# Optimization experiments

Hardware: AMD Instinct MI355X
Metric: run time of the kernel (lower is better)

## Reference

```python
import jax, jax.numpy as jnp
import numpy as np
import math

N_HEAD = 8
N_FEAT = 512
D_K = N_FEAT // N_HEAD
B, T = 4, 2048


def setup_inputs() -> dict:
    key = jax.random.key(0)
    ks = jax.random.split(key, 16)
    s = 1.0 / math.sqrt(N_FEAT)
    return {
        "x": jax.random.normal(ks[0], (B, T, N_FEAT), dtype=jnp.float32),
        "pos_emb": jax.random.normal(ks[1], (1, T, N_FEAT), dtype=jnp.float32),
        "Wq": jax.random.normal(ks[2], (N_FEAT, N_FEAT), dtype=jnp.float32) * s,
        "bq": jnp.zeros((N_FEAT,), dtype=jnp.float32),
        "Wk": jax.random.normal(ks[3], (N_FEAT, N_FEAT), dtype=jnp.float32) * s,
        "bk": jnp.zeros((N_FEAT,), dtype=jnp.float32),
        "Wv": jax.random.normal(ks[4], (N_FEAT, N_FEAT), dtype=jnp.float32) * s,
        "bv": jnp.zeros((N_FEAT,), dtype=jnp.float32),
        "Wpos": jax.random.normal(ks[5], (N_FEAT, N_FEAT), dtype=jnp.float32) * s,
        "Wout": jax.random.normal(ks[6], (N_FEAT, N_FEAT), dtype=jnp.float32) * s,
        "bout": jnp.zeros((N_FEAT,), dtype=jnp.float32),
        "pos_bias_u": jax.random.normal(ks[7], (N_HEAD, D_K), dtype=jnp.float32) * 0.05,
        "pos_bias_v": jax.random.normal(ks[8], (N_HEAD, D_K), dtype=jnp.float32) * 0.05,
    }


def reference(x, pos_emb, Wq, bq, Wk, bk, Wv, bv, Wpos, Wout, bout,
              pos_bias_u, pos_bias_v):
    b, t, f = x.shape
    h, d = N_HEAD, D_K
    # QKV projections (torch Linear: y = x @ W.T + b), split into heads -> (B,H,T,d)
    q = (jnp.einsum('btf,of->bto', x, Wq) + bq).reshape(b, t, h, d).transpose(0, 2, 1, 3)
    k = (jnp.einsum('btf,of->bto', x, Wk) + bk).reshape(b, t, h, d).transpose(0, 2, 1, 3)
    v = (jnp.einsum('btf,of->bto', x, Wv) + bv).reshape(b, t, h, d).transpose(0, 2, 1, 3)
    # positional projection: (1, T_pos, F) -> (H, T_pos, d)
    tp = pos_emb.shape[1]
    p = jnp.einsum('ptf,of->pto', pos_emb, Wpos).reshape(tp, h, d).transpose(1, 0, 2)
    q_u = q + pos_bias_u[None, :, None, :]  # (B,H,T,d)
    q_v = q + pos_bias_v[None, :, None, :]
    matrix_ac = jnp.einsum('bhtd,bhsd->bhts', q_u, k)   # content-content
    matrix_bd = jnp.einsum('bhtd,hsd->bhts', q_v, p)    # content-position
    scores = (matrix_ac + matrix_bd) / math.sqrt(d)
    attn = jax.nn.softmax(scores, axis=-1)  # dropout is identity in eval mode
    out = jnp.einsum('bhts,bhsd->bhtd', attn, v)
    out = out.transpose(0, 2, 1, 3).reshape(b, t, h * d)
    return jnp.einsum('btf,of->bto', out, Wout) + bout
```

## Files before the change

### kernel.cpp

```cpp
#include <hip/hip_runtime.h>

typedef float f4 __attribute__((ext_vector_type(4)));
typedef __attribute__((ext_vector_type(8))) short bf16x8;
typedef __attribute__((ext_vector_type(4))) float f32x4;
typedef __attribute__((ext_vector_type(2))) int i32x2;

#define T_SEQ 2048
#define NFEAT 512
#define NHEAD 8
#define DK    64
#define BATCH 4

using gptr_t = const __attribute__((address_space(1))) void*;
using lptr_t = __attribute__((address_space(3))) void*;

#define LOG2E_8 0.18033688011f


static __device__ __forceinline__ short f2bf(float f) {
    unsigned u = __builtin_bit_cast(unsigned, f);
    u += 0x7fff + ((u >> 16) & 1);
    return (short)(u >> 16);
}
static __device__ __forceinline__ float b2f(short s) {
    unsigned u = ((unsigned)(unsigned short)s) << 16;
    return __builtin_bit_cast(float, u);
}
static __device__ __forceinline__ int pkbf(float a, float b) {
    unsigned ua = __builtin_bit_cast(unsigned, a) + 0x8000u;
    unsigned ub = __builtin_bit_cast(unsigned, b) + 0x8000u;
    return (int)((ua >> 16) | (ub & 0xFFFF0000u));
}

__global__ __launch_bounds__(256) void cvt_kernel(
    const float* __restrict__ x, const float* __restrict__ pos,
    const float* __restrict__ Wq, const float* __restrict__ Wk, const float* __restrict__ Wv,
    const float* __restrict__ Wpos, const float* __restrict__ Wout,
    const float* __restrict__ bq, const float* __restrict__ bk, const float* __restrict__ bv,
    short* __restrict__ xb, short* __restrict__ posb, short* __restrict__ wqkv,
    short* __restrict__ wpb, short* __restrict__ wob, float* __restrict__ bqkv)
{
    const int blk = blockIdx.x;
    const float* src; short* dst; int off;
    if      (blk < 2048) { src = x;    dst = xb;          off = blk * 2048; }
    else if (blk < 2560) { src = pos;  dst = posb;        off = (blk - 2048) * 2048; }
    else if (blk < 2688) { src = Wq;   dst = wqkv;        off = (blk - 2560) * 2048; }
    else if (blk < 2816) { src = Wk;   dst = wqkv + 262144; off = (blk - 2688) * 2048; }
    else if (blk < 2944) { src = Wv;   dst = wqkv + 524288; off = (blk - 2816) * 2048; }
    else if (blk < 3072) { src = Wpos; dst = wpb;         off = (blk - 2944) * 2048; }
    else if (blk < 3200) { src = Wout; dst = wob;         off = (blk - 3072) * 2048; }
    else {
        int t = threadIdx.x;
        bqkv[t]        = bq[t];        bqkv[256 + t]  = bq[256 + t];
        bqkv[512 + t]  = bk[t];        bqkv[768 + t]  = bk[256 + t];
        bqkv[1024 + t] = bv[t];        bqkv[1280 + t] = bv[256 + t];
        return;
    }
    int i = off + threadIdx.x * 8;
    f4 a = *(const f4*)(src + i);
    f4 b = *(const f4*)(src + i + 4);
    bf16x8 o;
#pragma unroll
    for (int j = 0; j < 4; ++j) { o[j] = f2bf(a[j]); o[4 + j] = f2bf(b[j]); }
    *(bf16x8*)(dst + i) = o;
}

template<int OUT_BF16>
static __device__ __forceinline__ void gemm_tile(
    short* As, short* Bs,
    const short* __restrict__ A, const short* __restrict__ B,
    const float* __restrict__ bias, void* __restrict__ Cv,
    int N, int K, int row0, int col0)
{
    const int tid = threadIdx.x, lane = tid & 63, wave = tid >> 6;
    const int col = lane & 15, quad = lane >> 4;
    const int wm = (wave >> 1) * 64, wn = (wave & 1) * 64;
    const int rl = lane & 15;

    const short* Abase = A + (size_t)(row0 + wave * 32 + rl) * K + (lane >> 4) * 8;
    const short* Bbase = B + (size_t)(col0 + wave * 32 + rl) * K + (lane >> 4) * 8;

    f32x4 acc[4][4];
#pragma unroll
    for (int i = 0; i < 4; ++i)
#pragma unroll
        for (int j = 0; j < 4; ++j) acc[i][j] = (f32x4){0.f, 0.f, 0.f, 0.f};

    for (int k0 = 0; k0 < K; k0 += 64) {
        __syncthreads();
#pragma unroll
        for (int c = 0; c < 2; ++c)
#pragma unroll
            for (int hf = 0; hf < 2; ++hf) {
                __builtin_amdgcn_global_load_lds((gptr_t)(Abase + (size_t)(16 * c) * K + k0 + hf * 32),
                                                 (lptr_t)(As + wave * 2048 + c * 1024 + hf * 512), 16, 0, 0);
                __builtin_amdgcn_global_load_lds((gptr_t)(Bbase + (size_t)(16 * c) * K + k0 + hf * 32),
                                                 (lptr_t)(Bs + wave * 2048 + c * 1024 + hf * 512), 16, 0, 0);
            }
        __syncthreads();
#pragma unroll
        for (int kt = 0; kt < 2; ++kt) {
            bf16x8 af[4], bfr[4];
#pragma unroll
            for (int mt = 0; mt < 4; ++mt)
                af[mt] = *(const bf16x8*)&As[((wm >> 4) + mt) * 1024 + (kt * 4 + quad) * 128 + col * 8];
#pragma unroll
            for (int nt = 0; nt < 4; ++nt)
                bfr[nt] = *(const bf16x8*)&Bs[((wn >> 4) + nt) * 1024 + (kt * 4 + quad) * 128 + col * 8];
#pragma unroll
            for (int mt = 0; mt < 4; ++mt)
#pragma unroll
                for (int nt = 0; nt < 4; ++nt)
                    acc[mt][nt] = __builtin_amdgcn_mfma_f32_16x16x32_bf16(af[mt], bfr[nt], acc[mt][nt], 0, 0, 0);
        }
    }

    float bv4[4];
#pragma unroll
    for (int nt = 0; nt < 4; ++nt)
        bv4[nt] = bias ? bias[col0 + wn + nt * 16 + col] : 0.f;
#pragma unroll
    for (int mt = 0; mt < 4; ++mt)
#pragma unroll
        for (int reg = 0; reg < 4; ++reg) {
            int r = row0 + wm + mt * 16 + quad * 4 + reg;
#pragma unroll
            for (int nt = 0; nt < 4; ++nt) {
                int c = col0 + wn + nt * 16 + col;
                float v = acc[mt][nt][reg] + bv4[nt];
                if (OUT_BF16) ((short*)Cv)[(size_t)r * N + c] = f2bf(v);
                else          ((float*)Cv)[(size_t)r * N + c] = v;
            }
        }
}

__global__ __launch_bounds__(256) void gemm_qkv_pos(
    const short* __restrict__ xb, const short* __restrict__ wqkv,
    const float* __restrict__ bqkv, short* __restrict__ QKV,
    const short* __restrict__ posb, const short* __restrict__ wpb,
    short* __restrict__ Pm)
{
    __shared__ short As[8192], Bs[8192];
    const int bid = blockIdx.x;
    if (bid < 768) {
        const int xcd = bid & 7, s = bid >> 3;
        const int row = xcd * 8 + (s & 7), colt = s >> 3;
        gemm_tile<1>(As, Bs, xb, wqkv, bqkv, QKV, 1536, 512, row * 128, colt * 128);
    } else {
        const int t = bid - 768;
        gemm_tile<1>(As, Bs, posb, wpb, nullptr, Pm, 512, 512, (t / 4) * 128, (t % 4) * 128);
    }
}

__global__ __launch_bounds__(256) void gemm_out_kernel(
    const short* __restrict__ Op, const float* __restrict__ Lb,
    const short* __restrict__ B, const float* __restrict__ bias,
    float* __restrict__ C)
{
    __shared__ short As[8192], Bs[8192];
    const int bid = blockIdx.x;
    const int xcd = bid & 7, s = bid >> 3;
    const int row0 = (xcd * 8 + (s & 7)) * 128, col0 = (s >> 3) * 128;
    const int N = 512, K = 512;

    const int tid = threadIdx.x, lane = tid & 63, wave = tid >> 6;
    const int col = lane & 15, quad = lane >> 4;
    const int wm = (wave >> 1) * 64, wn = (wave & 1) * 64;
    const int rl = lane & 15;

    const short* Bbase = B + (size_t)(col0 + wave * 32 + rl) * K + quad * 8;
    const int rA0 = row0 + wave * 32 + rl;

    f32x4 acc[4][4];
#pragma unroll
    for (int i = 0; i < 4; ++i)
#pragma unroll
        for (int j = 0; j < 4; ++j) acc[i][j] = (f32x4){0.f, 0.f, 0.f, 0.f};

    for (int k0 = 0; k0 < K; k0 += 64) {
        const int h = k0 >> 6;
        __syncthreads();
#pragma unroll
        for (int c = 0; c < 2; ++c)
#pragma unroll
            for (int hf = 0; hf < 2; ++hf)
                __builtin_amdgcn_global_load_lds((gptr_t)(Bbase + (size_t)(16 * c) * K + k0 + hf * 32),
                                                 (lptr_t)(Bs + wave * 2048 + c * 1024 + hf * 512), 16, 0, 0);
#pragma unroll
        for (int c = 0; c < 2; ++c) {
            const int r  = rA0 + c * 16;
            const int t  = r & 2047;
            const int bh = (r >> 11) * 8 + h;
            const float l = Lb[bh * T_SEQ + t] + Lb[65536 + bh * T_SEQ + t];
            const float inv = 1.f / l;
#pragma unroll
            for (int hf = 0; hf < 2; ++hf) {
                const short* src = Op + (size_t)r * NFEAT + k0 + hf * 32 + quad * 8;
                bf16x8 o1 = *(const bf16x8*)src;
                bf16x8 o2 = *(const bf16x8*)(src + 4194304);
                bf16x8 oc;
#pragma unroll
                for (int j = 0; j < 8; ++j) oc[j] = f2bf((b2f(o1[j]) + b2f(o2[j])) * inv);
                *(bf16x8*)&As[wave * 2048 + c * 1024 + hf * 512 + lane * 8] = oc;
            }
        }
        __syncthreads();
#pragma unroll
        for (int kt = 0; kt < 2; ++kt) {
            bf16x8 af[4], bfr[4];
#pragma unroll
            for (int mt = 0; mt < 4; ++mt)
                af[mt] = *(const bf16x8*)&As[((wm >> 4) + mt) * 1024 + (kt * 4 + quad) * 128 + col * 8];
#pragma unroll
            for (int nt = 0; nt < 4; ++nt)
                bfr[nt] = *(const bf16x8*)&Bs[((wn >> 4) + nt) * 1024 + (kt * 4 + quad) * 128 + col * 8];
#pragma unroll
            for (int mt = 0; mt < 4; ++mt)
#pragma unroll
                for (int nt = 0; nt < 4; ++nt)
                    acc[mt][nt] = __builtin_amdgcn_mfma_f32_16x16x32_bf16(af[mt], bfr[nt], acc[mt][nt], 0, 0, 0);
        }
    }

    float bv4[4];
#pragma unroll
    for (int nt = 0; nt < 4; ++nt)
        bv4[nt] = bias[col0 + wn + nt * 16 + col];
#pragma unroll
    for (int mt = 0; mt < 4; ++mt)
#pragma unroll
        for (int reg = 0; reg < 4; ++reg) {
            int r = row0 + wm + mt * 16 + quad * 4 + reg;
#pragma unroll
            for (int nt = 0; nt < 4; ++nt) {
                int c = col0 + wn + nt * 16 + col;
                C[(size_t)r * N + c] = acc[mt][nt][reg] + bv4[nt];
            }
        }
}

__global__ __launch_bounds__(256) void kvprep_kernel(
    const short* __restrict__ qkv, const short* __restrict__ pm,
    const float* __restrict__ u, const float* __restrict__ vb,
    short* __restrict__ kp, short* __restrict__ vt, float* __restrict__ cb)
{
    __shared__ short tile[64][72];
    const int tid = threadIdx.x, lr = tid >> 2, lc = (tid & 3) * 16;
    const int bh = blockIdx.y, b = bh >> 3, h = bh & 7, s0 = blockIdx.x * 64;

    const short* kptr = qkv + (size_t)(b * T_SEQ + s0 + lr) * 1536 + 512 + h * DK + lc;
    const short* pptr = pm + (size_t)(s0 + lr) * NFEAT + h * DK + lc;
    const short* vptr = qkv + (size_t)(b * T_SEQ + s0 + lr) * 1536 + 1024 + h * DK + lc;
    bf16x8 k0_ = *(const bf16x8*)kptr,       k1_ = *(const bf16x8*)(kptr + 8);
    bf16x8 p0_ = *(const bf16x8*)pptr,       p1_ = *(const bf16x8*)(pptr + 8);
    bf16x8 v0_ = *(const bf16x8*)vptr,       v1_ = *(const bf16x8*)(vptr + 8);

    float c = 0.f;
    bf16x8 o0, o1;
#pragma unroll
    for (int j = 0; j < 8; ++j) {
        float kf = b2f(k0_[j]), pf = b2f(p0_[j]);
        o0[j] = f2bf(kf + pf);
        c += u[h * DK + lc + j] * kf + vb[h * DK + lc + j] * pf;
        float kf1 = b2f(k1_[j]), pf1 = b2f(p1_[j]);
        o1[j] = f2bf(kf1 + pf1);
        c += u[h * DK + lc + 8 + j] * kf1 + vb[h * DK + lc + 8 + j] * pf1;
    }
    short* kpd = kp + ((size_t)bh * T_SEQ + s0 + lr) * DK + lc;
    *(bf16x8*)kpd       = o0;
    *(bf16x8*)(kpd + 8) = o1;
    c += __shfl_xor(c, 1);
    c += __shfl_xor(c, 2);
    if ((tid & 3) == 0) cb[(size_t)bh * T_SEQ + s0 + lr] = LOG2E_8 * c;

    *(bf16x8*)&tile[lr][lc]     = v0_;
    *(bf16x8*)&tile[lr][lc + 8] = v1_;
    __syncthreads();
    short* dst = vt + (size_t)(bh * DK + lr) * T_SEQ + s0 + lc;
    bf16x8 t0_, t1_;
#pragma unroll
    for (int j = 0; j < 8; ++j) { t0_[j] = tile[lc + j][lr]; t1_[j] = tile[lc + 8 + j][lr]; }
    *(bf16x8*)dst       = t0_;
    *(bf16x8*)(dst + 8) = t1_;
}

__global__ __launch_bounds__(256, 4) void attn_kernel(
    const short* __restrict__ qkv, const short* __restrict__ kp,
    const short* __restrict__ vt, const float* __restrict__ cb,
    short* __restrict__ Op, float* __restrict__ Lb)
{
    __shared__ __align__(16) short KPs[64][72], Vts[64][72], Ps[4][32][72];
    __shared__ float cs[64];
    const int tid = threadIdx.x, lane = tid & 63, wave = tid >> 6;
    const int col = lane & 15, quad = lane >> 4;
    const int idx = blockIdx.x;
    const int xcd = idx & 7, slot = idx >> 3;
    const int half = slot & 1;
    const int t0 = ((slot >> 1) & 15) * 128;
    const int bh = (slot >> 5) * 8 + xcd;
    const int base = half * 1024;
    const int b = bh >> 3, h = bh & 7;

    bf16x8 qa[2][2];
#pragma unroll
    for (int g = 0; g < 2; ++g) {
        const short* qb = qkv + (size_t)(b * T_SEQ + t0 + wave * 32 + g * 16 + col) * 1536 + h * DK + quad * 8;
        qa[g][0] = *(const bf16x8*)qb;
        qa[g][1] = *(const bf16x8*)(qb + 32);
    }

    bf16x8 onesb;
#pragma unroll
    for (int j = 0; j < 8; ++j) onesb[j] = (short)0x3F80;

    const int lr  = tid >> 2;
    const int lcq = (tid & 3) * 16;
    const int rho = 4 * (lr & 15) + (lr >> 4);

    const short* kpbase = kp + (size_t)bh * T_SEQ * DK;
    const short* vtbase = vt + (size_t)bh * DK * T_SEQ;

    const short* kpp = kpbase + (size_t)(base + rho) * DK + lcq;
    const short* vtp = vtbase + (size_t)lr * T_SEQ + base + lcq;
    const float* cbp = cb + (size_t)bh * T_SEQ + base + tid;

    bf16x8 kpr0 = *(const bf16x8*)kpp;
    bf16x8 kpr1 = *(const bf16x8*)(kpp + 8);
    bf16x8 vtr0 = *(const bf16x8*)vtp;
    bf16x8 vtr1 = *(const bf16x8*)(vtp + 8);
    float cbr = (tid < 64) ? *cbp : 0.f;

    f32x4 Oacc[2][4];
    f32x4 Lacc[2];
#pragma unroll
    for (int g = 0; g < 2; ++g) {
        Lacc[g] = (f32x4){0.f, 0.f, 0.f, 0.f};
#pragma unroll
        for (int i = 0; i < 4; ++i) Oacc[g][i] = (f32x4){0.f, 0.f, 0.f, 0.f};
    }

    for (int it = 0; it < 16; ++it) {
        __syncthreads();
        *(bf16x8*)&KPs[lr][lcq]     = kpr0;
        *(bf16x8*)&KPs[lr][lcq + 8] = kpr1;
        *(bf16x8*)&Vts[lr][lcq]     = vtr0;
        *(bf16x8*)&Vts[lr][lcq + 8] = vtr1;
        if (tid < 64) cs[tid] = cbr;
        __syncthreads();

        kpp += 64 * DK; vtp += 64; cbp += 64;
        kpr0 = *(const bf16x8*)kpp;
        kpr1 = *(const bf16x8*)(kpp + 8);
        vtr0 = *(const bf16x8*)vtp;
        vtr1 = *(const bf16x8*)(vtp + 8);
        if (tid < 64) cbr = *cbp;

        f32x4 S[2][4];
#pragma unroll
        for (int g = 0; g < 2; ++g)
#pragma unroll
            for (int nt = 0; nt < 4; ++nt) S[g][nt] = (f32x4){0.f, 0.f, 0.f, 0.f};
#pragma unroll
        for (int nt = 0; nt < 4; ++nt) {
            bf16x8 b0 = *(const bf16x8*)&KPs[nt * 16 + col][quad * 8];
            bf16x8 b1 = *(const bf16x8*)&KPs[nt * 16 + col][32 + quad * 8];
            S[0][nt] = __builtin_amdgcn_mfma_f32_16x16x32_bf16(qa[0][0], b0, S[0][nt], 0, 0, 0);
            S[1][nt] = __builtin_amdgcn_mfma_f32_16x16x32_bf16(qa[1][0], b0, S[1][nt], 0, 0, 0);
            S[0][nt] = __builtin_amdgcn_mfma_f32_16x16x32_bf16(qa[0][1], b1, S[0][nt], 0, 0, 0);
            S[1][nt] = __builtin_amdgcn_mfma_f32_16x16x32_bf16(qa[1][1], b1, S[1][nt], 0, 0, 0);
        }
        const f4 cv = *(const f4*)&cs[4 * col];
#pragma unroll
        for (int g = 0; g < 2; ++g)
#pragma unroll
            for (int reg = 0; reg < 4; ++reg) {
                float e0 = __builtin_amdgcn_exp2f(fmaf(S[g][0][reg], LOG2E_8, cv[0]));
                float e1 = __builtin_amdgcn_exp2f(fmaf(S[g][1][reg], LOG2E_8, cv[1]));
                float e2 = __builtin_amdgcn_exp2f(fmaf(S[g][2][reg], LOG2E_8, cv[2]));
                float e3 = __builtin_amdgcn_exp2f(fmaf(S[g][3][reg], LOG2E_8, cv[3]));
                i32x2 pw; pw[0] = pkbf(e0, e1); pw[1] = pkbf(e2, e3);
                *(i32x2*)&Ps[wave][g * 16 + quad * 4 + reg][4 * col] = pw;
            }
#pragma unroll
        for (int kt = 0; kt < 2; ++kt) {
            bf16x8 pa0 = *(const bf16x8*)&Ps[wave][col][kt * 32 + quad * 8];
            bf16x8 pa1 = *(const bf16x8*)&Ps[wave][16 + col][kt * 32 + quad * 8];
            Lacc[0] = __builtin_amdgcn_mfma_f32_16x16x32_bf16(pa0, onesb, Lacc[0], 0, 0, 0);
            Lacc[1] = __builtin_amdgcn_mfma_f32_16x16x32_bf16(pa1, onesb, Lacc[1], 0, 0, 0);
#pragma unroll
            for (int dt = 0; dt < 4; ++dt) {
                bf16x8 vb = *(const bf16x8*)&Vts[dt * 16 + col][kt * 32 + quad * 8];
                Oacc[0][dt] = __builtin_amdgcn_mfma_f32_16x16x32_bf16(pa0, vb, Oacc[0][dt], 0, 0, 0);
                Oacc[1][dt] = __builtin_amdgcn_mfma_f32_16x16x32_bf16(pa1, vb, Oacc[1][dt], 0, 0, 0);
            }
        }
    }
    short* ophalf = Op + (size_t)half * 4194304;
    float* lhalf  = Lb + (size_t)half * 65536 + (size_t)bh * T_SEQ;
#pragma unroll
    for (int g = 0; g < 2; ++g)
#pragma unroll
        for (int reg = 0; reg < 4; ++reg) {
            int t = t0 + wave * 32 + g * 16 + quad * 4 + reg;
            if (col == 0) lhalf[t] = Lacc[g][reg];
            short* op = ophalf + (size_t)(b * T_SEQ + t) * NFEAT + h * DK;
#pragma unroll
            for (int dt = 0; dt < 4; ++dt)
                op[dt * 16 + col] = f2bf(Oacc[g][dt][reg]);
        }
}

extern "C" void kernel_launch(void* const* d_in, const int* in_sizes, int n_in,
                              void* d_out, int out_size, void* d_ws, size_t ws_size,
                              hipStream_t stream)
{
    const float* x    = (const float*)d_in[0];
    const float* pos  = (const float*)d_in[1];
    const float* Wq   = (const float*)d_in[2];
    const float* bq   = (const float*)d_in[3];
    const float* Wk   = (const float*)d_in[4];
    const float* bk   = (const float*)d_in[5];
    const float* Wv   = (const float*)d_in[6];
    const float* bv   = (const float*)d_in[7];
    const float* Wpos = (const float*)d_in[8];
    const float* Wout = (const float*)d_in[9];
    const float* bout = (const float*)d_in[10];
    const float* pbu  = (const float*)d_in[11];
    const float* pbv  = (const float*)d_in[12];
    float* out = (float*)d_out;

    short* xb   = (short*)d_ws;
    short* posb = xb   + 4194304;
    short* wqkv = posb + 1048576;
    short* wpb  = wqkv + 786432;
    short* wob  = wpb  + 262144;
    short* QKV  = wob  + 262144;
    short* Pm   = QKV  + 12582912;
    short* KP   = Pm   + 1048576;
    short* Vt   = KP   + 4194304;
    short* AttO = Vt   + 4194304;
    float* bqkv = (float*)(AttO + 4194304);
    float* Cb   = bqkv + 1536;
    short* Op   = (short*)(Cb + 65536);
    float* Lb   = (float*)(Op + 8388608);

    cvt_kernel<<<dim3(3201), dim3(256), 0, stream>>>(x, pos, Wq, Wk, Wv, Wpos, Wout, bq, bk, bv,
                                                     xb, posb, wqkv, wpb, wob, bqkv);
    gemm_qkv_pos<<<dim3(832), dim3(256), 0, stream>>>(xb, wqkv, bqkv, QKV, posb, wpb, Pm);
    kvprep_kernel<<<dim3(T_SEQ / 64, BATCH * NHEAD), dim3(256), 0, stream>>>(QKV, Pm, pbu, pbv, KP, Vt, Cb);
    attn_kernel<<<dim3(1024), dim3(256), 0, stream>>>(QKV, KP, Vt, Cb, Op, Lb);
    gemm_out_kernel<<<dim3(256), dim3(256), 0, stream>>>(Op, Lb, wob, bout, out);
}
```

Baseline: 215.0 us.

## Keep softmax probabilities in registers by transposing MFMA operands in attention

The attention kernel swaps MFMA operand order so it computes S transposed (keys as A, queries as B). The exponentiated probabilities then land in a register layout that can feed the P·V MFMA directly, with no round trip through the per-wave Ps shared-memory buffer. To keep the result correct, the K/P rows and column biases are loaded with a permuted row index (kap) that matches the new register ordering. The epilogue now writes packed 4-element bf16 outputs per lane instead of scalar stores, and it drops the shared-memory write/read and part of the LDS footprint. The risk is in the index permutation: if it does not match the MFMA layout, the scores are silently wrong.

```diff
diff --git a/kernel.cpp b/kernel.cpp
--- a/kernel.cpp
+++ b/kernel.cpp
@@ -4,6 +4,7 @@
 typedef __attribute__((ext_vector_type(8))) short bf16x8;
 typedef __attribute__((ext_vector_type(4))) float f32x4;
 typedef __attribute__((ext_vector_type(2))) int i32x2;
+typedef __attribute__((ext_vector_type(4))) int i32x4;
 
 #define T_SEQ 2048
 #define NFEAT 512
@@ -29,6 +30,11 @@
 static __device__ __forceinline__ int pkbf(float a, float b) {
     unsigned ua = __builtin_bit_cast(unsigned, a) + 0x8000u;
     unsigned ub = __builtin_bit_cast(unsigned, b) + 0x8000u;
+    return (int)((ua >> 16) | (ub & 0xFFFF0000u));
+}
+static __device__ __forceinline__ int pkbf_rne(float a, float b) {
+    unsigned ua = __builtin_bit_cast(unsigned, a); ua += 0x7fff + ((ua >> 16) & 1);
+    unsigned ub = __builtin_bit_cast(unsigned, b); ub += 0x7fff + ((ub >> 16) & 1);
     return (int)((ua >> 16) | (ub & 0xFFFF0000u));
 }
 
@@ -289,7 +295,7 @@
     const short* __restrict__ vt, const float* __restrict__ cb,
     short* __restrict__ Op, float* __restrict__ Lb)
 {
-    __shared__ __align__(16) short KPs[64][72], Vts[64][72], Ps[4][32][72];
+    __shared__ __align__(16) short KPs[64][72], Vts[64][72];
     __shared__ float cs[64];
     const int tid = threadIdx.x, lane = tid & 63, wave = tid >> 6;
     const int col = lane & 15, quad = lane >> 4;
@@ -315,14 +321,15 @@
 
     const int lr  = tid >> 2;
     const int lcq = (tid & 3) * 16;
-    const int rho = 4 * (lr & 15) + (lr >> 4);
+    const int kap  = (lr & 32) | ((lr & 12) << 1) | ((lr & 16) >> 2) | (lr & 3);
+    const int kapt = (tid & 32) | ((tid & 12) << 1) | ((tid & 16) >> 2) | (tid & 3);
 
     const short* kpbase = kp + (size_t)bh * T_SEQ * DK;
     const short* vtbase = vt + (size_t)bh * DK * T_SEQ;
 
-    const short* kpp = kpbase + (size_t)(base + rho) * DK + lcq;
+    const short* kpp = kpbase + (size_t)(base + kap) * DK + lcq;
     const short* vtp = vtbase + (size_t)lr * T_SEQ + base + lcq;
-    const float* cbp = cb + (size_t)bh * T_SEQ + base + tid;
+    const float* cbp = cb + (size_t)bh * T_SEQ + base + kapt;
 
     bf16x8 kpr0 = *(const bf16x8*)kpp;
     bf16x8 kpr1 = *(const bf16x8*)(kpp + 8);
@@ -362,52 +369,58 @@
             for (int nt = 0; nt < 4; ++nt) S[g][nt] = (f32x4){0.f, 0.f, 0.f, 0.f};
 #pragma unroll
         for (int nt = 0; nt < 4; ++nt) {
-            bf16x8 b0 = *(const bf16x8*)&KPs[nt * 16 + col][quad * 8];
-            bf16x8 b1 = *(const bf16x8*)&KPs[nt * 16 + col][32 + quad * 8];
-            S[0][nt] = __builtin_amdgcn_mfma_f32_16x16x32_bf16(qa[0][0], b0, S[0][nt], 0, 0, 0);
-            S[1][nt] = __builtin_amdgcn_mfma_f32_16x16x32_bf16(qa[1][0], b0, S[1][nt], 0, 0, 0);
-            S[0][nt] = __builtin_amdgcn_mfma_f32_16x16x32_bf16(qa[0][1], b1, S[0][nt], 0, 0, 0);
-            S[1][nt] = __builtin_amdgcn_mfma_f32_16x16x32_bf16(qa[1][1], b1, S[1][nt], 0, 0, 0);
-        }
-        const f4 cv = *(const f4*)&cs[4 * col];
-#pragma unroll
-        for (int g = 0; g < 2; ++g)
-#pragma unroll
-            for (int reg = 0; reg < 4; ++reg) {
-                float e0 = __builtin_amdgcn_exp2f(fmaf(S[g][0][reg], LOG2E_8, cv[0]));
-                float e1 = __builtin_amdgcn_exp2f(fmaf(S[g][1][reg], LOG2E_8, cv[1]));
-                float e2 = __builtin_amdgcn_exp2f(fmaf(S[g][2][reg], LOG2E_8, cv[2]));
-                float e3 = __builtin_amdgcn_exp2f(fmaf(S[g][3][reg], LOG2E_8, cv[3]));
-                i32x2 pw; pw[0] = pkbf(e0, e1); pw[1] = pkbf(e2, e3);
-                *(i32x2*)&Ps[wave][g * 16 + quad * 4 + reg][4 * col] = pw;
-            }
+            bf16x8 a0 = *(const bf16x8*)&KPs[nt * 16 + col][quad * 8];
+            bf16x8 a1 = *(const bf16x8*)&KPs[nt * 16 + col][32 + quad * 8];
+            S[0][nt] = __builtin_amdgcn_mfma_f32_16x16x32_bf16(a0, qa[0][0], S[0][nt], 0, 0, 0);
+            S[1][nt] = __builtin_amdgcn_mfma_f32_16x16x32_bf16(a0, qa[1][0], S[1][nt], 0, 0, 0);
+            S[0][nt] = __builtin_amdgcn_mfma_f32_16x16x32_bf16(a1, qa[0][1], S[0][nt], 0, 0, 0);
+            S[1][nt] = __builtin_amdgcn_mfma_f32_16x16x32_bf16(a1, qa[1][1], S[1][nt], 0, 0, 0);
+        }
+        int pk_[2][4][2];
+#pragma unroll
+        for (int nt = 0; nt < 4; ++nt) {
+            const f4 cvn = *(const f4*)&cs[nt * 16 + quad * 4];
+#pragma unroll
+            for (int g = 0; g < 2; ++g) {
+                float e0 = __builtin_amdgcn_exp2f(fmaf(S[g][nt][0], LOG2E_8, cvn[0]));
+                float e1 = __builtin_amdgcn_exp2f(fmaf(S[g][nt][1], LOG2E_8, cvn[1]));
+                float e2 = __builtin_amdgcn_exp2f(fmaf(S[g][nt][2], LOG2E_8, cvn[2]));
+                float e3 = __builtin_amdgcn_exp2f(fmaf(S[g][nt][3], LOG2E_8, cvn[3]));
+                pk_[g][nt][0] = pkbf(e0, e1);
+                pk_[g][nt][1] = pkbf(e2, e3);
+            }
+        }
 #pragma unroll
         for (int kt = 0; kt < 2; ++kt) {
-            bf16x8 pa0 = *(const bf16x8*)&Ps[wave][col][kt * 32 + quad * 8];
-            bf16x8 pa1 = *(const bf16x8*)&Ps[wave][16 + col][kt * 32 + quad * 8];
-            Lacc[0] = __builtin_amdgcn_mfma_f32_16x16x32_bf16(pa0, onesb, Lacc[0], 0, 0, 0);
-            Lacc[1] = __builtin_amdgcn_mfma_f32_16x16x32_bf16(pa1, onesb, Lacc[1], 0, 0, 0);
+            i32x4 w0 = (i32x4){pk_[0][2 * kt][0], pk_[0][2 * kt][1], pk_[0][2 * kt + 1][0], pk_[0][2 * kt + 1][1]};
+            i32x4 w1 = (i32x4){pk_[1][2 * kt][0], pk_[1][2 * kt][1], pk_[1][2 * kt + 1][0], pk_[1][2 * kt + 1][1]};
+            bf16x8 pf0 = __builtin_bit_cast(bf16x8, w0);
+            bf16x8 pf1 = __builtin_bit_cast(bf16x8, w1);
+            Lacc[0] = __builtin_amdgcn_mfma_f32_16x16x32_bf16(onesb, pf0, Lacc[0], 0, 0, 0);
+            Lacc[1] = __builtin_amdgcn_mfma_f32_16x16x32_bf16(onesb, pf1, Lacc[1], 0, 0, 0);
 #pragma unroll
             for (int dt = 0; dt < 4; ++dt) {
                 bf16x8 vb = *(const bf16x8*)&Vts[dt * 16 + col][kt * 32 + quad * 8];
-                Oacc[0][dt] = __builtin_amdgcn_mfma_f32_16x16x32_bf16(pa0, vb, Oacc[0][dt], 0, 0, 0);
-                Oacc[1][dt] = __builtin_amdgcn_mfma_f32_16x16x32_bf16(pa1, vb, Oacc[1][dt], 0, 0, 0);
+                Oacc[0][dt] = __builtin_amdgcn_mfma_f32_16x16x32_bf16(vb, pf0, Oacc[0][dt], 0, 0, 0);
+                Oacc[1][dt] = __builtin_amdgcn_mfma_f32_16x16x32_bf16(vb, pf1, Oacc[1][dt], 0, 0, 0);
             }
         }
     }
     short* ophalf = Op + (size_t)half * 4194304;
     float* lhalf  = Lb + (size_t)half * 65536 + (size_t)bh * T_SEQ;
 #pragma unroll
-    for (int g = 0; g < 2; ++g)
-#pragma unroll
-        for (int reg = 0; reg < 4; ++reg) {
-            int t = t0 + wave * 32 + g * 16 + quad * 4 + reg;
-            if (col == 0) lhalf[t] = Lacc[g][reg];
-            short* op = ophalf + (size_t)(b * T_SEQ + t) * NFEAT + h * DK;
-#pragma unroll
-            for (int dt = 0; dt < 4; ++dt)
-                op[dt * 16 + col] = f2bf(Oacc[g][dt][reg]);
-        }
+    for (int g = 0; g < 2; ++g) {
+        const int t = t0 + wave * 32 + g * 16 + col;
+        if (quad == 0) lhalf[t] = Lacc[g][0];
+        short* op = ophalf + (size_t)(b * T_SEQ + t) * NFEAT + h * DK;
+#pragma unroll
+        for (int dt = 0; dt < 4; ++dt) {
+            i32x2 w;
+            w[0] = pkbf_rne(Oacc[g][dt][0], Oacc[g][dt][1]);
+            w[1] = pkbf_rne(Oacc[g][dt][2], Oacc[g][dt][3]);
+            *(i32x2*)(op + dt * 16 + quad * 4) = w;
+        }
+    }
 }
 
 extern "C" void kernel_launch(void* const* d_in, const int* in_sizes, int n_in,
```

Result: no change. 217.0 us (+1.0%).
